# Kernel optimization log

Measured on AMD Instinct MI355X. Metric: run time of the kernel, lower is better.

## Reference

```python
import jax, jax.numpy as jnp
import numpy as np

# NTU RGB+D 25-joint skeleton edges (1-based)
NTU_EDGES = [(1,2),(2,21),(3,21),(4,3),(5,21),(6,5),(7,6),(8,7),(9,21),(10,9),
             (11,10),(12,11),(13,1),(14,13),(15,14),(16,15),(17,1),(18,17),
             (19,18),(20,19),(22,23),(23,8),(24,25),(25,12)]
NUM_SCALES = 13
NUM_POINT = 25


def build_A_powers(num_scales=NUM_SCALES, v=NUM_POINT):
    # MS-G3D disentangled multi-scale aggregation: exact-k-hop adjacencies, each
    # with self loops, symmetrically normalized, stacked along dim 0 -> (K*V, V).
    A = np.zeros((v, v))
    for i, j in NTU_EDGES:
        A[i - 1, j - 1] = 1.0
        A[j - 1, i - 1] = 1.0
    I = np.eye(v)
    mats = []
    for k in range(num_scales):
        if k == 0:
            Ak = I.copy()
        else:
            Ak = np.minimum(np.linalg.matrix_power(A + I, k), 1) \
               - np.minimum(np.linalg.matrix_power(A + I, k - 1), 1)
            Ak = Ak + I  # with_self=True
        d = Ak.sum(-1)
        dinv = np.where(d > 0, d ** -0.5, 0.0)
        mats.append((dinv[:, None] * Ak) * dinv[None, :])
    return np.concatenate(mats, 0).astype(np.float32)


def batchnorm(x, g, b, axes, ch_axis, eps=1e-5):
    # torch BatchNorm in training mode: biased batch stats + affine
    mean = jnp.mean(x, axes, keepdims=True)
    var = jnp.mean((x - mean) ** 2, axes, keepdims=True)
    shape = [1] * x.ndim
    shape[ch_axis] = -1
    return (x - mean) * jax.lax.rsqrt(var + eps) * g.reshape(shape) + b.reshape(shape)


def ms_gcn(x, A_powers, A_res, W, b, g, beta, num_scales):
    # x: (N, C, T, V); A: (K*V, V)
    A = A_powers + A_res
    support = jnp.einsum('vu,nctu->nctv', A, x)            # (N, C, T, K*V)
    N, C, T, KV = support.shape
    V = KV // num_scales
    support = support.reshape(N, C, T, num_scales, V).transpose(0, 3, 1, 2, 4)
    support = support.reshape(N, num_scales * C, T, V)     # (N, K*C, T, V)
    out = jnp.einsum('oc,nctv->notv', W, support) + b[None, :, None, None]  # 1x1 conv
    out = batchnorm(out, g, beta, (0, 2, 3), 1)
    return jax.nn.relu(out)


def lstm(x, Wih, Whh, bih, bhh):
    # single-layer batch_first LSTM, zero initial state; torch gate order i,f,g,o
    B = x.shape[0]
    H = Whh.shape[1]
    xp = jnp.einsum('bsd,hd->bsh', x, Wih) + bih + bhh     # precompute input proj

    def step(carry, xt):
        h, c = carry
        gates = xt + h @ Whh.T
        i, f, g, o = jnp.split(gates, 4, axis=-1)
        c = jax.nn.sigmoid(f) * c + jax.nn.sigmoid(i) * jnp.tanh(g)
        h = jax.nn.sigmoid(o) * jnp.tanh(c)
        return (h, c), h

    init = (jnp.zeros((B, H), x.dtype), jnp.zeros((B, H), x.dtype))
    _, ys = jax.lax.scan(step, init, jnp.swapaxes(xp, 0, 1))
    return jnp.swapaxes(ys, 0, 1)                          # (B, S, H)


def logsig_rnn(x, n_segments, Wih, Whh, bih, bhh):
    # x: (B, T, d). Depth-2 log-signature per time segment + segment start point,
    # concatenated and fed to an LSTM (Logsig-RNN layer).
    B, T, d = x.shape
    t_vec = np.array([int(round(float(v))) for v in np.linspace(1, T, n_segments + 1)])
    starts = t_vec[:-1] - 1
    ends = t_vec[1:] - 1
    L = int((ends - starts).max()) + 1
    # pad segments to fixed length by repeating the last point (zero increments)
    idx = np.minimum(starts[:, None] + np.arange(L)[None, :], ends[:, None])  # (S, L)
    pts = x[:, idx, :]                                     # (B, S, L, d)
    rel = pts - pts[:, :, :1, :]
    inc = rel[:, :, -1, :]                                 # level-1: total increment
    dx = pts[:, :, 1:, :] - pts[:, :, :-1, :]
    Mm = jnp.einsum('bsli,bslj->bsij', rel[:, :, :-1, :], dx)
    iu, ju = np.triu_indices(d, k=1)
    levy = 0.5 * (Mm[:, :, iu, ju] - Mm[:, :, ju, iu])     # level-2 (Lyndon basis)
    feats = jnp.concatenate([x[:, starts, :], inc, levy], axis=-1)
    return lstm(feats, Wih, Whh, bih, bhh)


def setup_inputs() -> dict:
    key = jax.random.key(0)
    ks = iter(jax.random.split(key, 16))
    N, C, T, V, M = 2, 3, 100, 25, 2
    c1, c2, num_class, K = 96, 192, 60, NUM_SCALES

    def randn(shape, scale):
        return jax.random.normal(next(ks), shape, jnp.float32) * scale

    ls1 = c1 + c1 * (c1 - 1) // 2     # 4656
    ls2 = c2 + c2 * (c2 - 1) // 2     # 18528
    in1 = c1 + ls1                    # 4752
    in2 = c2 + ls2                    # 18720
    Ap = jnp.asarray(build_A_powers())
    return {
        'x': jax.random.normal(next(ks), (N, C, T, V, M), jnp.float32),
        'length': jax.random.randint(next(ks), (N,), 0, T),
        'data_bn_g': jnp.ones((M * V * C,)), 'data_bn_b': jnp.zeros((M * V * C,)),
        'A_powers1': Ap,
        'A_res1': jax.random.uniform(next(ks), Ap.shape, jnp.float32, -1e-6, 1e-6),
        'W1': randn((c1, K * C), (K * C) ** -0.5), 'b1': jnp.zeros((c1,)),
        'bn1_g': jnp.ones((c1,)), 'bn1_b': jnp.zeros((c1,)),
        'Wih1': randn((4 * c1, in1), in1 ** -0.5), 'Whh1': randn((4 * c1, c1), c1 ** -0.5),
        'bih1': jnp.zeros((4 * c1,)), 'bhh1': jnp.zeros((4 * c1,)),
        'bnseg1_g': jnp.ones((50,)), 'bnseg1_b': jnp.zeros((50,)),
        'A_powers2': Ap,
        'A_res2': jax.random.uniform(next(ks), Ap.shape, jnp.float32, -1e-6, 1e-6),
        'W2': randn((c2, K * c1), (K * c1) ** -0.5), 'b2': jnp.zeros((c2,)),
        'bn2_g': jnp.ones((c2,)), 'bn2_b': jnp.zeros((c2,)),
        'Wih2': randn((4 * c2, in2), in2 ** -0.5), 'Whh2': randn((4 * c2, c2), c2 ** -0.5),
        'bih2': jnp.zeros((4 * c2,)), 'bhh2': jnp.zeros((4 * c2,)),
        'bnseg2_g': jnp.ones((30,)), 'bnseg2_b': jnp.zeros((30,)),
        'fcW': randn((num_class, c2), c2 ** -0.5), 'fcb': jnp.zeros((num_class,)),
    }


def reference(x, length, data_bn_g, data_bn_b, A_powers1, A_res1, W1, b1, bn1_g, bn1_b,
              Wih1, Whh1, bih1, bhh1, bnseg1_g, bnseg1_b, A_powers2, A_res2, W2, b2,
              bn2_g, bn2_b, Wih2, Whh2, bih2, bhh2, bnseg2_g, bnseg2_b, fcW, fcb):
    # `length` is accepted but unused, as in the original forward.
    N, C, T, V, M = x.shape
    K = A_powers1.shape[0] // V
    c1, c2 = W1.shape[0], W2.shape[0]
    S1, S2 = 50, 30

    h = x.transpose(0, 4, 3, 1, 2).reshape(N, M * V * C, T)
    h = batchnorm(h, data_bn_g, data_bn_b, (0, 2), 1)
    h = h.reshape(N * M, V, C, T).transpose(0, 2, 3, 1)            # (NM, C, T, V)

    h = jax.nn.relu(ms_gcn(h, A_powers1, A_res1, W1, b1, bn1_g, bn1_b, K))
    h = h.transpose(0, 3, 2, 1).reshape(N * M * V, T, c1)
    h = logsig_rnn(h, S1, Wih1, Whh1, bih1, bhh1)                  # (NMV, S1, c1)
    h = batchnorm(h, bnseg1_g, bnseg1_b, (0, 2), 1)
    h = h.reshape(N * M, V, S1, c1).transpose(0, 3, 2, 1)          # (NM, c1, S1, V)

    h = jax.nn.relu(ms_gcn(h, A_powers2, A_res2, W2, b2, bn2_g, bn2_b, K))
    h = h.transpose(0, 3, 2, 1).reshape(N * M * V, S1, c2)
    h = logsig_rnn(h, S2, Wih2, Whh2, bih2, bhh2)                  # (NMV, S2, c2)
    h = batchnorm(h, bnseg2_g, bnseg2_b, (0, 2), 1)
    h = h.reshape(N * M, V, S2, c2).transpose(0, 3, 2, 1)          # (NM, c2, S2, V)

    pooled = h.reshape(N, M, c2, -1).mean(axis=3).mean(axis=1)     # (N, c2)
    return pooled @ fcW.T + fcb
```

## Files before the change

kernel.cpp:

```cpp
#include <hip/hip_runtime.h>
#include <cmath>
#include <cstdint>
#include <cstddef>

typedef unsigned short bf16_t;
typedef __attribute__((ext_vector_type(8))) short short8;
typedef __attribute__((ext_vector_type(4))) float floatx4;
typedef __attribute__((ext_vector_type(2))) _Float16 half2_t;

__device__ __forceinline__ float bf2f(bf16_t b){
  unsigned int u = ((unsigned int)b) << 16;
  return __uint_as_float(u);
}
__device__ __forceinline__ bf16_t f2bf(float f){
  unsigned int u = __float_as_uint(f);
  unsigned int r = (u + 0x7fffu + ((u >> 16) & 1u)) >> 16;
  return (bf16_t)r;
}
__device__ __forceinline__ unsigned int f2bf2(float a, float b){
  return (unsigned int)f2bf(a) | ((unsigned int)f2bf(b) << 16);
}
__device__ __forceinline__ float sigf(float x){ return 1.0f / (1.0f + expf(-x)); }

__device__ __forceinline__ float dot2(half2_t a, half2_t b, float c){
#if __has_builtin(__builtin_amdgcn_fdot2)
  return __builtin_amdgcn_fdot2(a, b, c, false);
#else
  return c + (float)a.x * (float)b.x + (float)a.y * (float)b.y;
#endif
}

__device__ __forceinline__ void gload_lds16(const bf16_t* g, bf16_t* lds){
  __builtin_amdgcn_global_load_lds(
      (const __attribute__((address_space(1))) unsigned int*)g,
      (__attribute__((address_space(3))) unsigned int*)lds, 16, 0, 0);
}

__global__ void prep_misc(const float* __restrict__ a1, const float* __restrict__ r1, float* __restrict__ o1,
                          const float* __restrict__ a2, const float* __restrict__ r2, float* __restrict__ o2,
                          const float* __restrict__ bi1, const float* __restrict__ bh1, float* __restrict__ ob1,
                          const float* __restrict__ bi2, const float* __restrict__ bh2, float* __restrict__ ob2,
                          const float* __restrict__ Whh1, half2_t* __restrict__ Wp1,
                          const float* __restrict__ Whh2, half2_t* __restrict__ Wp2,
                          unsigned short* __restrict__ lut1, unsigned short* __restrict__ lut2,
                          float* __restrict__ stats, bf16_t* __restrict__ A2mat){
  int i = blockIdx.x * blockDim.x + threadIdx.x;
  if (i < 8125){ o1[i] = a1[i] + r1[i]; o2[i] = a2[i] + r2[i]; }
  if (i < 384) ob1[i] = bi1[i] + bh1[i];
  if (i < 768) ob2[i] = bi2[i] + bh2[i];
  if (i < 736) stats[i] = 0.f;
  if (i < 18432){
    int t = i % 384, j2 = i / 384;
    half2_t w; w.x = (_Float16)Whh1[(size_t)t * 96 + 2 * j2];
    w.y = (_Float16)Whh1[(size_t)t * 96 + 2 * j2 + 1];
    Wp1[i] = w;
  }
  if (i < 73728){
    int t = i % 768, j2 = i / 768;
    half2_t w; w.x = (_Float16)Whh2[(size_t)t * 192 + 2 * j2];
    w.y = (_Float16)Whh2[(size_t)t * 192 + 2 * j2 + 1];
    Wp2[i] = w;
  }
  if (i < 4560){
    int d = 96, p = i;
    int r = (int)(((2.0 * d - 1.0) - sqrt((2.0 * d - 1.0) * (2.0 * d - 1.0) - 8.0 * (double)p)) * 0.5);
    if (r < 0) r = 0;
    while (r + 1 <= d - 2 && (r + 1) * (d - 1) - ((r + 1) * r) / 2 <= p) ++r;
    while (r > 0 && r * (d - 1) - (r * (r - 1)) / 2 > p) --r;
    int jj = p - (r * (d - 1) - (r * (r - 1)) / 2);
    lut1[p] = (unsigned short)((r << 8) | (r + 1 + jj));
  }
  if (i < 18336){
    int d = 192, p = i;
    int r = (int)(((2.0 * d - 1.0) - sqrt((2.0 * d - 1.0) * (2.0 * d - 1.0) - 8.0 * (double)p)) * 0.5);
    if (r < 0) r = 0;
    while (r + 1 <= d - 2 && (r + 1) * (d - 1) - ((r + 1) * r) / 2 <= p) ++r;
    while (r > 0 && r * (d - 1) - (r * (r - 1)) / 2 > p) --r;
    int jj = p - (r * (d - 1) - (r * (r - 1)) / 2);
    lut2[p] = (unsigned short)((r << 8) | (r + 1 + jj));
  }
  if (i < 160000){
    int row = i >> 5, col = 1248 + (i & 31);
    A2mat[(size_t)row * 1280 + col] = 0;
  }
}

__device__ __forceinline__ void f2bf_seg(const float* in, bf16_t* out, int Kin, int Kout, int li){
  int ko8 = Kout >> 3;
  int r = li / ko8, k8 = (li % ko8) << 3;
  uint4 u;
  if (k8 + 8 <= Kin){
    const float4* p = reinterpret_cast<const float4*>(in + (size_t)r * Kin + k8);
    float4 x0 = p[0], x1 = p[1];
    u.x = f2bf2(x0.x, x0.y); u.y = f2bf2(x0.z, x0.w);
    u.z = f2bf2(x1.x, x1.y); u.w = f2bf2(x1.z, x1.w);
  } else {
    u.x = u.y = u.z = u.w = 0u;
  }
  *reinterpret_cast<uint4*>(out + (size_t)r * Kout + k8) = u;
}

__global__ void f2bf_pad8_3(const float* __restrict__ in1, bf16_t* __restrict__ out1, int Kin1, int Kout1, int c1,
                            const float* __restrict__ in2, bf16_t* __restrict__ out2, int Kin2, int Kout2, int c2,
                            const float* __restrict__ in3, bf16_t* __restrict__ out3, int Kin3, int Kout3, int c3){
  int idx = blockIdx.x * blockDim.x + threadIdx.x;
  if (idx < c1){ f2bf_seg(in1, out1, Kin1, Kout1, idx); return; }
  idx -= c1;
  if (idx < c2){ f2bf_seg(in2, out2, Kin2, Kout2, idx); return; }
  idx -= c2;
  if (idx < c3) f2bf_seg(in3, out3, Kin3, Kout3, idx);
}

__global__ void data_bn_kernel(const float* __restrict__ x, const float* __restrict__ g,
                               const float* __restrict__ bb, float* __restrict__ h1,
                               int N, int C, int T, int V, int M){
  int ch = blockIdx.x;
  int m = ch / (V * C);
  int v = (ch / C) % V;
  int c = ch % C;
  int tid = threadIdx.x;
  int cnt = N * T;
  float s = 0.f, s2 = 0.f;
  for (int i = tid; i < cnt; i += 64){
    int n = i / T, t = i % T;
    float val = x[(((size_t)(n * C + c) * T + t) * V + v) * M + m];
    s += val; s2 += val * val;
  }
  for (int off = 32; off; off >>= 1){ s += __shfl_down(s, off); s2 += __shfl_down(s2, off); }
  s = __shfl(s, 0); s2 = __shfl(s2, 0);
  float mean = s / cnt;
  float rstd = rsqrtf(s2 / cnt - mean * mean + 1e-5f);
  float gg = g[ch], bo = bb[ch];
  for (int i = tid; i < cnt; i += 64){
    int n = i / T, t = i % T;
    float val = x[(((size_t)(n * C + c) * T + t) * V + v) * M + m];
    float y = (val - mean) * rstd * gg + bo;
    h1[((size_t)((n * M + m) * C + c) * T + t) * V + v] = y;
  }
}

__global__ void support1_kernel(const float* __restrict__ A, const float* __restrict__ hin,
                                float* __restrict__ sup, int total){
  int idx = blockIdx.x * blockDim.x + threadIdx.x;
  if (idx >= total) return;
  int w = idx % 325;
  int rest = idx / 325;
  const float* row = hin + (size_t)rest * 25;
  const float* ar = A + w * 25;
  float acc = 0.f;
  #pragma unroll
  for (int u = 0; u < 25; ++u) acc += ar[u] * row[u];
  sup[idx] = acc;
}

__global__ void gcn1_out_kernel(const float* __restrict__ sup, const float* __restrict__ W1,
                                const float* __restrict__ b1, float* __restrict__ y1, int NM, int T){
  int idx = blockIdx.x * blockDim.x + threadIdx.x;
  int total = NM * T * 25 * 96;
  if (idx >= total) return;
  int o = idx % 96;
  int v = (idx / 96) % 25;
  int t = (idx / (96 * 25)) % T;
  int nm = idx / (96 * 25 * T);
  float acc = b1[o];
  #pragma unroll
  for (int k = 0; k < 13; ++k)
    #pragma unroll
    for (int c = 0; c < 3; ++c)
      acc += W1[o * 39 + k * 3 + c] * sup[(size_t)((nm * 3 + c) * T + t) * 325 + k * 25 + v];
  y1[idx] = acc;
}

__global__ void colstats_atomic(const float* __restrict__ mat, int R,
                                float* __restrict__ sum, float* __restrict__ sumsq){
  int col = threadIdx.x;
  int Cc = blockDim.x;
  float s = 0.f, s2 = 0.f;
  for (int r = blockIdx.x; r < R; r += gridDim.x){
    float v = mat[(size_t)r * Cc + col];
    s += v; s2 += v * v;
  }
  atomicAdd(&sum[col], s);
  atomicAdd(&sumsq[col], s2);
}

__global__ void segstats_atomic(const float* __restrict__ lout, int R2, int S,
                                float* __restrict__ sum, float* __restrict__ sumsq){
  int t = threadIdx.x;
  int H = blockDim.x;
  int nw = H >> 6;
  __shared__ float ra[4], rb[4];
  int lane = t & 63, wid = t >> 6;
  for (int r = blockIdx.x; r < R2; r += gridDim.x){
    int s = r % S;
    float v = lout[(size_t)r * H + t];
    float a = v, b2 = v * v;
    for (int off = 32; off; off >>= 1){ a += __shfl_down(a, off); b2 += __shfl_down(b2, off); }
    if (lane == 0){ ra[wid] = a; rb[wid] = b2; }
    __syncthreads();
    if (t == 0){
      float sa = 0.f, sb = 0.f;
      for (int w = 0; w < nw; ++w){ sa += ra[w]; sb += rb[w]; }
      atomicAdd(&sum[s], sa);
      atomicAdd(&sumsq[s], sb);
    }
    __syncthreads();
  }
}

__global__ void bn_relu_seq_kernel(const float* __restrict__ ymat, const float* __restrict__ sum,
                                   const float* __restrict__ sumsq, const float* __restrict__ g,
                                   const float* __restrict__ bb, float* __restrict__ xseq,
                                   int NM, int T, int H, int R){
  int idx = blockIdx.x * blockDim.x + threadIdx.x;
  int total = NM * T * 25 * H;
  if (idx >= total) return;
  int o = idx % H;
  int v = (idx / H) % 25;
  int t = (idx / (H * 25)) % T;
  int nm = idx / (H * 25 * T);
  float mean = sum[o] / R;
  float rstd = rsqrtf(sumsq[o] / R - mean * mean + 1e-5f);
  float val = (ymat[idx] - mean) * rstd * g[o] + bb[o];
  val = fmaxf(val, 0.f);
  int b = nm * 25 + v;
  xseq[((size_t)b * T + t) * H + o] = val;
}

struct SegTable { int st[50]; int en[50]; };

__global__ void feats_kernel(const float* __restrict__ xseq, bf16_t* __restrict__ feats,
                             SegTable segs, const unsigned int* __restrict__ lut32,
                             int T, int d, int S, int L, int pairs, int rowlenP){
  __shared__ float pts[4][192];
  int bs = blockIdx.x;
  int b = bs / S, s = bs % S;
  int st = segs.st[s], en = segs.en[s];
  int nt = blockDim.x, tid = threadIdx.x;
  for (int l = 0; l < L; ++l){
    int t = st + l; if (t > en) t = en;
    for (int i = tid; i < d; i += nt) pts[l][i] = xseq[((size_t)b * T + t) * d + i];
  }
  __syncthreads();
  unsigned int* frow32 = reinterpret_cast<unsigned int*>(feats + (size_t)bs * rowlenP);
  int d2 = d >> 1;
  for (int i2 = tid; i2 < d2; i2 += nt){
    int i = 2 * i2;
    frow32[i2]      = f2bf2(pts[0][i], pts[0][i + 1]);
    frow32[d2 + i2] = f2bf2(pts[L - 1][i] - pts[0][i], pts[L - 1][i + 1] - pts[0][i + 1]);
  }
  int rowlen2 = (2 * d + pairs) >> 1, rowlenP2 = rowlenP >> 1;
  for (int i = tid + rowlen2; i < rowlenP2; i += nt) frow32[i] = 0;
  int Lm2 = L - 2;
  unsigned int* lrow32 = frow32 + d;
  int pairs2 = pairs >> 1;
  for (int p2 = tid; p2 < pairs2; p2 += nt){
    unsigned int ee = lut32[p2];
    int i0 = (ee >> 8) & 255, j0 = ee & 255;
    int i1 = ee >> 24, j1 = (ee >> 16) & 255;
    float acc0 = 0.f, acc1 = 0.f;
    for (int l = 1; l <= Lm2; ++l){
      float p0i = pts[0][i0], p0j = pts[0][j0], p0i1 = pts[0][i1], p0j1 = pts[0][j1];
      float ri = pts[l][i0] - p0i, rj = pts[l][j0] - p0j;
      float di = pts[l + 1][i0] - pts[l][i0], dj = pts[l + 1][j0] - pts[l][j0];
      acc0 += ri * dj - rj * di;
      float ri1 = pts[l][i1] - p0i1, rj1 = pts[l][j1] - p0j1;
      float di1 = pts[l + 1][i1] - pts[l][i1], dj1 = pts[l + 1][j1] - pts[l][j1];
      acc1 += ri1 * dj1 - rj1 * di1;
    }
    lrow32[p2] = f2bf2(0.5f * acc0, 0.5f * acc1);
  }
}

__global__ __launch_bounds__(256)
void gemm_mfma_nt_split(const bf16_t* __restrict__ A, const bf16_t* __restrict__ B,
                        float* __restrict__ P, int M, int N, int K){
  __shared__ bf16_t As[128 * 64];
  __shared__ bf16_t Bs[128 * 64];
  const int tid = threadIdx.x;
  const int lane = tid & 63, wv = tid >> 6;
  const int bm = blockIdx.x * 128, bn = blockIdx.y * 128;
  const int wr = (wv >> 1) * 64, wc = (wv & 1) * 64;
  const int m_l = lane & 15, q = lane >> 4;

  const int ksteps = K >> 6;
  const int Z = gridDim.z, z = blockIdx.z;
  const int per = (ksteps + Z - 1) / Z;
  const int ks0 = z * per;
  const int ks1 = (ks0 + per < ksteps) ? ks0 + per : ksteps;

  const int rlane = lane >> 3;
  const int slane = lane & 7;
  const int colc = (slane ^ rlane) * 8;
  const bf16_t* gA[4]; const bf16_t* gB[4];
  bf16_t* lA[4]; bf16_t* lB[4];
  #pragma unroll
  for (int it = 0; it < 4; ++it){
    int c = it * 4 + wv;
    int rowA = bm + c * 8 + rlane; if (rowA > M - 1) rowA = M - 1;
    int rowB = bn + c * 8 + rlane; if (rowB > N - 1) rowB = N - 1;
    gA[it] = A + (size_t)rowA * K + colc;
    gB[it] = B + (size_t)rowB * K + colc;
    lA[it] = &As[c * 512];
    lB[it] = &Bs[c * 512];
  }
  const int sxor = m_l & 7;

  floatx4 acc[4][4] = {};
  for (int ks = ks0; ks < ks1; ++ks){
    int k0 = ks << 6;
    __syncthreads();
    #pragma unroll
    for (int it = 0; it < 4; ++it){
      gload_lds16(gA[it] + k0, lA[it]);
      gload_lds16(gB[it] + k0, lB[it]);
    }
    __syncthreads();
    #pragma unroll
    for (int half = 0; half < 2; ++half){
      const int scol = ((half * 4 + q) ^ sxor) * 8;
      short8 af[4], bfr[4];
      #pragma unroll
      for (int i = 0; i < 4; ++i){
        af[i]  = *reinterpret_cast<const short8*>(&As[(wr + i * 16 + m_l) * 64 + scol]);
        bfr[i] = *reinterpret_cast<const short8*>(&Bs[(wc + i * 16 + m_l) * 64 + scol]);
      }
      #pragma unroll
      for (int mi = 0; mi < 4; ++mi)
        #pragma unroll
        for (int ni = 0; ni < 4; ++ni)
          acc[mi][ni] = __builtin_amdgcn_mfma_f32_16x16x32_bf16(af[mi], bfr[ni], acc[mi][ni], 0, 0, 0);
    }
  }

  float* Pz = P + (size_t)z * M * N;
  #pragma unroll
  for (int mi = 0; mi < 4; ++mi){
    int row0 = bm + wr + mi * 16 + q * 4;
    #pragma unroll
    for (int r = 0; r < 4; ++r){
      int row = row0 + r;
      if (row < M){
        #pragma unroll
        for (int ni = 0; ni < 4; ++ni){
          int col = bn + wc + ni * 16 + m_l;
          if (col < N) Pz[(size_t)row * N + col] = acc[mi][ni][r];
        }
      }
    }
  }
}

__global__ void reduce_split_bias(const float* __restrict__ P, const float* __restrict__ bias,
                                  float* __restrict__ out, int MN, int N, int Z){
  int i4 = (blockIdx.x * blockDim.x + threadIdx.x) * 4;
  if (i4 >= MN) return;
  const float4 bv = *reinterpret_cast<const float4*>(bias + (i4 % N));
  float4 s = bv;
  for (int z = 0; z < Z; ++z){
    const float4 p = *reinterpret_cast<const float4*>(P + (size_t)z * MN + i4);
    s.x += p.x; s.y += p.y; s.z += p.z; s.w += p.w;
  }
  *reinterpret_cast<float4*>(out + i4) = s;
}

template <int H2C, int BLK, int Z>
__global__ __launch_bounds__(BLK)
void lstm_kernel(const float* __restrict__ P, const float* __restrict__ bias,
                 const half2_t* __restrict__ Wp, float* __restrict__ out,
                 int S, int MN){
  constexpr int H = 2 * H2C;
  constexpr int H4 = 4 * H;
  __shared__ _Float16 __attribute__((aligned(16))) hsh[H];
  __shared__ float gv[H4];
  const int b = blockIdx.x, t = threadIdx.x;
  half2_t w[H2C];
  const half2_t* wp = Wp + t;
  #pragma unroll
  for (int j2 = 0; j2 < H2C; ++j2) w[j2] = wp[(size_t)j2 * H4];
  float cc = 0.f;
  if (t < H) hsh[t] = (_Float16)0.f;
  const float bval = bias[t];
  const size_t base = (size_t)b * S * H4 + t;
  float pv0[Z], pv1[Z];
  #pragma unroll
  for (int z = 0; z < Z; ++z) pv0[z] = P[(size_t)z * MN + base];
  #pragma unroll
  for (int z = 0; z < Z; ++z) pv1[z] = P[(size_t)z * MN + base + H4];
  __syncthreads();
  const half2_t* hp = reinterpret_cast<const half2_t*>(hsh);
  for (int s = 0; s < S; ++s){
    float pvn[Z];
    if (s + 2 < S){
      size_t o2 = base + (size_t)(s + 2) * H4;
      #pragma unroll
      for (int z = 0; z < Z; ++z) pvn[z] = P[(size_t)z * MN + o2];
    }
    float a0 = bval, a1 = 0.f, a2 = 0.f, a3 = 0.f;
    float a4 = 0.f, a5 = 0.f, a6 = 0.f, a7 = 0.f;
    #pragma unroll
    for (int z = 0; z < Z; ++z) a0 += pv0[z];
    #pragma unroll
    for (int j2 = 0; j2 < H2C; j2 += 8){
      a0 = dot2(w[j2],     hp[j2],     a0);
      a1 = dot2(w[j2 + 1], hp[j2 + 1], a1);
      a2 = dot2(w[j2 + 2], hp[j2 + 2], a2);
      a3 = dot2(w[j2 + 3], hp[j2 + 3], a3);
      a4 = dot2(w[j2 + 4], hp[j2 + 4], a4);
      a5 = dot2(w[j2 + 5], hp[j2 + 5], a5);
      a6 = dot2(w[j2 + 6], hp[j2 + 6], a6);
      a7 = dot2(w[j2 + 7], hp[j2 + 7], a7);
    }
    gv[t] = ((a0 + a1) + (a2 + a3)) + ((a4 + a5) + (a6 + a7));
    __syncthreads();
    if (t < H){
      float ig = sigf(gv[t]);
      float fg = sigf(gv[H + t]);
      float gg = tanhf(gv[2 * H + t]);
      float og = sigf(gv[3 * H + t]);
      cc = fg * cc + ig * gg;
      float hh = og * tanhf(cc);
      hsh[t] = (_Float16)hh;
      out[((size_t)b * S + s) * H + t] = hh;
    }
    __syncthreads();
    #pragma unroll
    for (int z = 0; z < Z; ++z){ pv0[z] = pv1[z]; pv1[z] = pvn[z]; }
  }
}

__global__ void bnseg_to_g2in_kernel(const float* __restrict__ lout, const float* __restrict__ sum,
                                     const float* __restrict__ sumsq, const float* __restrict__ g,
                                     const float* __restrict__ bb, float* __restrict__ g2in,
                                     int B, int S, int H, int cnt){
  int idx = blockIdx.x * blockDim.x + threadIdx.x;
  int total = B * S * H;
  if (idx >= total) return;
  int hh = idx % H;
  int s = (idx / H) % S;
  int b = idx / (H * S);
  float mean = sum[s] / cnt;
  float rstd = rsqrtf(sumsq[s] / cnt - mean * mean + 1e-5f);
  float val = (lout[idx] - mean) * rstd * g[s] + bb[s];
  int nm = b / 25, v = b % 25;
  g2in[(((size_t)(nm * S + s) * 25 + v) * H) + hh] = val;
}

__global__ void support2_kernel(const float* __restrict__ A, const float* __restrict__ g2in,
                                bf16_t* __restrict__ A2mat, int NM, int C1, int S){
  int idx = blockIdx.x * blockDim.x + threadIdx.x;
  int total = NM * S * 25 * 13 * 96;
  if (idx >= total) return;
  int c = idx % 96;
  int k = (idx / 96) % 13;
  int v = (idx / (96 * 13)) % 25;
  int rs = idx / (96 * 13 * 25);
  const float* gbase = g2in + ((size_t)rs * 25) * 96 + c;
  const float* ar = A + (k * 25 + v) * 25;
  float acc = 0.f;
  #pragma unroll
  for (int u = 0; u < 25; ++u) acc += ar[u] * gbase[(size_t)u * 96];
  A2mat[((size_t)rs * 25 + v) * 1280 + k * 96 + c] = f2bf(acc);
}

__global__ void pool_kernel(const float* __restrict__ lout2, const float* __restrict__ sum,
                            const float* __restrict__ sumsq, const float* __restrict__ g,
                            const float* __restrict__ bb, float* __restrict__ pooled,
                            int S, int H, int scnt){
  int n = blockIdx.x / H;
  int o = blockIdx.x % H;
  float acc = 0.f;
  int cnt = 2 * 25 * S;
  for (int i = threadIdx.x; i < cnt; i += 64){
    int m = i / (25 * S);
    int r = i % (25 * S);
    int v = r / S;
    int s = r % S;
    int b = (n * 2 + m) * 25 + v;
    float val = lout2[((size_t)b * S + s) * H + o];
    float mean = sum[s] / scnt;
    float rstd = rsqrtf(sumsq[s] / scnt - mean * mean + 1e-5f);
    val = (val - mean) * rstd * g[s] + bb[s];
    acc += val;
  }
  for (int off = 32; off; off >>= 1) acc += __shfl_down(acc, off);
  if (threadIdx.x == 0) pooled[n * H + o] = acc / cnt;
}

__global__ void fc_kernel(const float* __restrict__ pooled, const float* __restrict__ fcW,
                          const float* __restrict__ fcb, float* __restrict__ outp){
  int idx = blockIdx.x * blockDim.x + threadIdx.x;
  if (idx >= 120) return;
  int n = idx / 60, cls = idx % 60;
  float acc = fcb[cls];
  for (int o = 0; o < 192; ++o) acc += pooled[n * 192 + o] * fcW[cls * 192 + o];
  outp[idx] = acc;
}

static void make_segs(int T, int S, SegTable& tab, int& L){
  double step = (double)(T - 1) / (double)S;
  long long tv[51];
  for (int i = 0; i <= S; ++i){
    double v = 1.0 + step * (double)i;
    tv[i] = llrint(v);
  }
  L = 0;
  for (int s = 0; s < S; ++s){
    tab.st[s] = (int)tv[s] - 1;
    tab.en[s] = (int)tv[s + 1] - 1;
    int len = tab.en[s] - tab.st[s] + 1;
    if (len > L) L = len;
  }
  for (int s = S; s < 50; ++s){ tab.st[s] = 0; tab.en[s] = 0; }
  if (L > 4) L = 4;
}

extern "C" void kernel_launch(void* const* d_in, const int* in_sizes, int n_in,
                              void* d_out, int out_size, void* d_ws, size_t ws_size,
                              hipStream_t stream){
  const float* x         = (const float*)d_in[0];
  const float* data_bn_g = (const float*)d_in[2];
  const float* data_bn_b = (const float*)d_in[3];
  const float* A_powers1 = (const float*)d_in[4];
  const float* A_res1    = (const float*)d_in[5];
  const float* W1        = (const float*)d_in[6];
  const float* b1        = (const float*)d_in[7];
  const float* bn1_g     = (const float*)d_in[8];
  const float* bn1_b     = (const float*)d_in[9];
  const float* Wih1      = (const float*)d_in[10];
  const float* Whh1      = (const float*)d_in[11];
  const float* bih1      = (const float*)d_in[12];
  const float* bhh1      = (const float*)d_in[13];
  const float* bnseg1_g  = (const float*)d_in[14];
  const float* bnseg1_b  = (const float*)d_in[15];
  const float* A_powers2 = (const float*)d_in[16];
  const float* A_res2    = (const float*)d_in[17];
  const float* W2        = (const float*)d_in[18];
  const float* b2        = (const float*)d_in[19];
  const float* bn2_g     = (const float*)d_in[20];
  const float* bn2_b     = (const float*)d_in[21];
  const float* Wih2      = (const float*)d_in[22];
  const float* Whh2      = (const float*)d_in[23];
  const float* bih2      = (const float*)d_in[24];
  const float* bhh2      = (const float*)d_in[25];
  const float* bnseg2_g  = (const float*)d_in[26];
  const float* bnseg2_b  = (const float*)d_in[27];
  const float* fcW       = (const float*)d_in[28];
  const float* fcb       = (const float*)d_in[29];
  float* out = (float*)d_out;

  const int N = 2, C = 3, T = 100, V = 25, M = 2, NM = 4;
  const int K = 13, C1 = 96, C2 = 192;
  const int S1 = 50, S2 = 30;
  const int B = 100;
  const int IN1 = 4752, IN2 = 18720;
  const int IN1P = 4800, IN2P = 18752;
  const int P1 = 4560, P2 = 18336;
  const int KG2 = 1248, KG2P = 1280;
  const int Z1 = 5, Z2 = 6, ZG = 4;

  size_t off = 0;
  char* base = (char*)d_ws;
  auto alloc = [&](size_t nbytes) -> void* {
    off = (off + 255) & ~(size_t)255;
    void* p = base + off;
    off += nbytes;
    return p;
  };
  float* A1full = (float*)alloc(325 * 25 * 4);
  float* A2full = (float*)alloc(325 * 25 * 4);
  float* h1     = (float*)alloc((size_t)NM * C * T * V * 4);
  float* sup1   = (float*)alloc((size_t)NM * C * T * 325 * 4);
  float* y1mat  = (float*)alloc((size_t)NM * T * V * C1 * 4);
  float* stats  = (float*)alloc(736 * 4);
  float* st1a = stats, *st1b = stats + 96;
  float* sg1a = stats + 192, *sg1b = stats + 242;
  float* st2a = stats + 292, *st2b = stats + 484;
  float* sg2a = stats + 676, *sg2b = stats + 706;
  float* xseq1  = (float*)alloc((size_t)B * T * C1 * 4);
  float* l1out  = (float*)alloc((size_t)B * S1 * C1 * 4);
  float* g2in   = (float*)alloc((size_t)NM * S1 * V * C1 * 4);
  bf16_t* A2mat = (bf16_t*)alloc((size_t)NM * S1 * V * KG2P * 2);
  float* y2mat  = (float*)alloc((size_t)NM * S1 * V * C2 * 4);
  float* xseq2  = (float*)alloc((size_t)B * S1 * C2 * 4);
  float* l2out  = (float*)alloc((size_t)B * S2 * C2 * 4);
  float* pooled = (float*)alloc(2 * C2 * 4);
  float* bias1  = (float*)alloc(4 * C1 * 4);
  float* bias2  = (float*)alloc(4 * C2 * 4);
  half2_t* Wp1  = (half2_t*)alloc((size_t)(C1 / 2) * 4 * C1 * 4);
  half2_t* Wp2  = (half2_t*)alloc((size_t)(C2 / 2) * 4 * C2 * 4);
  bf16_t* Wih1b = (bf16_t*)alloc((size_t)4 * C1 * IN1P * 2);
  bf16_t* Wih2b = (bf16_t*)alloc((size_t)4 * C2 * IN2P * 2);
  bf16_t* W2b   = (bf16_t*)alloc((size_t)C2 * KG2P * 2);
  unsigned short* lut1 = (unsigned short*)alloc((size_t)P1 * 2);
  unsigned short* lut2 = (unsigned short*)alloc((size_t)P2 * 2);
  size_t pmax = (size_t)Z2 * 3000 * 768;
  {
    size_t p1s = (size_t)Z1 * 5000 * 384; if (p1s > pmax) pmax = p1s;
    size_t pgs = (size_t)ZG * 5000 * 192; if (pgs > pmax) pmax = pgs;
  }
  float* Pbuf = (float*)alloc(pmax * 4);
  bf16_t* feats = (bf16_t*)alloc((size_t)B * S2 * IN2P * 2);
  (void)ws_size; (void)in_sizes; (void)n_in; (void)out_size;

  prep_misc<<<625, 256, 0, stream>>>(A_powers1, A_res1, A1full, A_powers2, A_res2, A2full,
                                     bih1, bhh1, bias1, bih2, bhh2, bias2,
                                     Whh1, Wp1, Whh2, Wp2, lut1, lut2, stats, A2mat);
  {
    int c1 = 4 * C1 * (IN1P / 8);
    int c2 = 4 * C2 * (IN2P / 8);
    int c3 = C2 * (KG2P / 8);
    int tot = c1 + c2 + c3;
    f2bf_pad8_3<<<(tot + 255) / 256, 256, 0, stream>>>(Wih1, Wih1b, IN1, IN1P, c1,
                                                       Wih2, Wih2b, IN2, IN2P, c2,
                                                       W2, W2b, KG2, KG2P, c3);
  }

  data_bn_kernel<<<M * V * C, 64, 0, stream>>>(x, data_bn_g, data_bn_b, h1, N, C, T, V, M);

  int tot_sup1 = NM * C * T * 325;
  support1_kernel<<<(tot_sup1 + 255) / 256, 256, 0, stream>>>(A1full, h1, sup1, tot_sup1);
  int tot_y1 = NM * T * 25 * C1;
  gcn1_out_kernel<<<(tot_y1 + 255) / 256, 256, 0, stream>>>(sup1, W1, b1, y1mat, NM, T);
  colstats_atomic<<<256, C1, 0, stream>>>(y1mat, NM * T * 25, st1a, st1b);
  bn_relu_seq_kernel<<<(tot_y1 + 255) / 256, 256, 0, stream>>>(y1mat, st1a, st1b, bn1_g, bn1_b,
                                                               xseq1, NM, T, C1, NM * T * 25);

  SegTable seg1, seg2; int L1, L2;
  make_segs(T, S1, seg1, L1);
  make_segs(S1, S2, seg2, L2);

  feats_kernel<<<B * S1, 256, 0, stream>>>(xseq1, feats, seg1, (const unsigned int*)lut1,
                                           T, C1, S1, L1, P1, IN1P);
  {
    int Mm = B * S1, Nn = 4 * C1;
    dim3 g((Mm + 127) / 128, (Nn + 127) / 128, Z1);
    gemm_mfma_nt_split<<<g, 256, 0, stream>>>(feats, Wih1b, Pbuf, Mm, Nn, IN1P);
    lstm_kernel<48, 384, Z1><<<B, 384, 0, stream>>>(Pbuf, bias1, Wp1, l1out, S1, Mm * Nn);
  }
  segstats_atomic<<<256, C1, 0, stream>>>(l1out, B * S1, S1, sg1a, sg1b);
  int tot_bn1 = B * S1 * C1;
  bnseg_to_g2in_kernel<<<(tot_bn1 + 255) / 256, 256, 0, stream>>>(l1out, sg1a, sg1b, bnseg1_g,
                                                                  bnseg1_b, g2in, B, S1, C1, B * C1);

  int tot_sup2 = NM * S1 * 25 * 13 * 96;
  support2_kernel<<<(tot_sup2 + 255) / 256, 256, 0, stream>>>(A2full, g2in, A2mat, NM, C1, S1);
  {
    int Mm = NM * S1 * 25, Nn = C2;
    dim3 g((Mm + 127) / 128, (Nn + 127) / 128, ZG);
    gemm_mfma_nt_split<<<g, 256, 0, stream>>>(A2mat, W2b, Pbuf, Mm, Nn, KG2P);
    int MN = Mm * Nn;
    reduce_split_bias<<<(MN / 4 + 255) / 256, 256, 0, stream>>>(Pbuf, b2, y2mat, MN, Nn, ZG);
  }
  colstats_atomic<<<256, C2, 0, stream>>>(y2mat, NM * S1 * 25, st2a, st2b);
  int tot_y2 = NM * S1 * 25 * C2;
  bn_relu_seq_kernel<<<(tot_y2 + 255) / 256, 256, 0, stream>>>(y2mat, st2a, st2b, bn2_g, bn2_b,
                                                               xseq2, NM, S1, C2, NM * S1 * 25);

  feats_kernel<<<B * S2, 256, 0, stream>>>(xseq2, feats, seg2, (const unsigned int*)lut2,
                                           S1, C2, S2, L2, P2, IN2P);
  {
    int Mm = B * S2, Nn = 4 * C2;
    dim3 g((Mm + 127) / 128, (Nn + 127) / 128, Z2);
    gemm_mfma_nt_split<<<g, 256, 0, stream>>>(feats, Wih2b, Pbuf, Mm, Nn, IN2P);
    lstm_kernel<96, 768, Z2><<<B, 768, 0, stream>>>(Pbuf, bias2, Wp2, l2out, S2, Mm * Nn);
  }
  segstats_atomic<<<256, C2, 0, stream>>>(l2out, B * S2, S2, sg2a, sg2b);

  pool_kernel<<<2 * C2, 64, 0, stream>>>(l2out, sg2a, sg2b, bnseg2_g, bnseg2_b, pooled, S2, C2, B * C2);
  fc_kernel<<<1, 128, 0, stream>>>(pooled, fcW, fcb, out);
}
```

Before: 706.7 us.

## Fuse GCN, batchnorm stats and weight conversion into neighbouring kernels

Merges support1, gcn1_out and its column stats into one per-(nm,t) block kernel. Folds the BN+ReLU application into the feature kernel, the segment stats into the LSTM step loop, and the segment BN into support2. Moves the fp32-to-bf16 weight conversion into the GEMM B-tile load, and computes GCN2 stats during the split-K reduction. The aim is to cut many launches and intermediate buffers, at the cost of redundant per-call weight conversion inside the GEMM and extra shared atomics.

```diff
diff --git a/kernel.cpp b/kernel.cpp
--- a/kernel.cpp
+++ b/kernel.cpp
@@ -85,32 +85,6 @@
   }
 }
 
-__device__ __forceinline__ void f2bf_seg(const float* in, bf16_t* out, int Kin, int Kout, int li){
-  int ko8 = Kout >> 3;
-  int r = li / ko8, k8 = (li % ko8) << 3;
-  uint4 u;
-  if (k8 + 8 <= Kin){
-    const float4* p = reinterpret_cast<const float4*>(in + (size_t)r * Kin + k8);
-    float4 x0 = p[0], x1 = p[1];
-    u.x = f2bf2(x0.x, x0.y); u.y = f2bf2(x0.z, x0.w);
-    u.z = f2bf2(x1.x, x1.y); u.w = f2bf2(x1.z, x1.w);
-  } else {
-    u.x = u.y = u.z = u.w = 0u;
-  }
-  *reinterpret_cast<uint4*>(out + (size_t)r * Kout + k8) = u;
-}
-
-__global__ void f2bf_pad8_3(const float* __restrict__ in1, bf16_t* __restrict__ out1, int Kin1, int Kout1, int c1,
-                            const float* __restrict__ in2, bf16_t* __restrict__ out2, int Kin2, int Kout2, int c2,
-                            const float* __restrict__ in3, bf16_t* __restrict__ out3, int Kin3, int Kout3, int c3){
-  int idx = blockIdx.x * blockDim.x + threadIdx.x;
-  if (idx < c1){ f2bf_seg(in1, out1, Kin1, Kout1, idx); return; }
-  idx -= c1;
-  if (idx < c2){ f2bf_seg(in2, out2, Kin2, Kout2, idx); return; }
-  idx -= c2;
-  if (idx < c3) f2bf_seg(in3, out3, Kin3, Kout3, idx);
-}
-
 __global__ void data_bn_kernel(const float* __restrict__ x, const float* __restrict__ g,
                                const float* __restrict__ bb, float* __restrict__ h1,
                                int N, int C, int T, int V, int M){
@@ -139,107 +113,68 @@
   }
 }
 
-__global__ void support1_kernel(const float* __restrict__ A, const float* __restrict__ hin,
-                                float* __restrict__ sup, int total){
-  int idx = blockIdx.x * blockDim.x + threadIdx.x;
-  if (idx >= total) return;
-  int w = idx % 325;
-  int rest = idx / 325;
-  const float* row = hin + (size_t)rest * 25;
-  const float* ar = A + w * 25;
-  float acc = 0.f;
-  #pragma unroll
-  for (int u = 0; u < 25; ++u) acc += ar[u] * row[u];
-  sup[idx] = acc;
-}
-
-__global__ void gcn1_out_kernel(const float* __restrict__ sup, const float* __restrict__ W1,
-                                const float* __restrict__ b1, float* __restrict__ y1, int NM, int T){
-  int idx = blockIdx.x * blockDim.x + threadIdx.x;
-  int total = NM * T * 25 * 96;
-  if (idx >= total) return;
-  int o = idx % 96;
-  int v = (idx / 96) % 25;
-  int t = (idx / (96 * 25)) % T;
-  int nm = idx / (96 * 25 * T);
-  float acc = b1[o];
-  #pragma unroll
-  for (int k = 0; k < 13; ++k)
-    #pragma unroll
-    for (int c = 0; c < 3; ++c)
-      acc += W1[o * 39 + k * 3 + c] * sup[(size_t)((nm * 3 + c) * T + t) * 325 + k * 25 + v];
-  y1[idx] = acc;
-}
-
-__global__ void colstats_atomic(const float* __restrict__ mat, int R,
-                                float* __restrict__ sum, float* __restrict__ sumsq){
-  int col = threadIdx.x;
-  int Cc = blockDim.x;
-  float s = 0.f, s2 = 0.f;
-  for (int r = blockIdx.x; r < R; r += gridDim.x){
-    float v = mat[(size_t)r * Cc + col];
-    s += v; s2 += v * v;
-  }
-  atomicAdd(&sum[col], s);
-  atomicAdd(&sumsq[col], s2);
-}
-
-__global__ void segstats_atomic(const float* __restrict__ lout, int R2, int S,
-                                float* __restrict__ sum, float* __restrict__ sumsq){
-  int t = threadIdx.x;
-  int H = blockDim.x;
-  int nw = H >> 6;
-  __shared__ float ra[4], rb[4];
-  int lane = t & 63, wid = t >> 6;
-  for (int r = blockIdx.x; r < R2; r += gridDim.x){
-    int s = r % S;
-    float v = lout[(size_t)r * H + t];
-    float a = v, b2 = v * v;
-    for (int off = 32; off; off >>= 1){ a += __shfl_down(a, off); b2 += __shfl_down(b2, off); }
-    if (lane == 0){ ra[wid] = a; rb[wid] = b2; }
-    __syncthreads();
-    if (t == 0){
-      float sa = 0.f, sb = 0.f;
-      for (int w = 0; w < nw; ++w){ sa += ra[w]; sb += rb[w]; }
-      atomicAdd(&sum[s], sa);
-      atomicAdd(&sumsq[s], sb);
-    }
-    __syncthreads();
-  }
-}
-
-__global__ void bn_relu_seq_kernel(const float* __restrict__ ymat, const float* __restrict__ sum,
-                                   const float* __restrict__ sumsq, const float* __restrict__ g,
-                                   const float* __restrict__ bb, float* __restrict__ xseq,
-                                   int NM, int T, int H, int R){
-  int idx = blockIdx.x * blockDim.x + threadIdx.x;
-  int total = NM * T * 25 * H;
-  if (idx >= total) return;
-  int o = idx % H;
-  int v = (idx / H) % 25;
-  int t = (idx / (H * 25)) % T;
-  int nm = idx / (H * 25 * T);
-  float mean = sum[o] / R;
-  float rstd = rsqrtf(sumsq[o] / R - mean * mean + 1e-5f);
-  float val = (ymat[idx] - mean) * rstd * g[o] + bb[o];
-  val = fmaxf(val, 0.f);
-  int b = nm * 25 + v;
-  xseq[((size_t)b * T + t) * H + o] = val;
+__global__ __launch_bounds__(256)
+void gcn1_fused(const float* __restrict__ A, const float* __restrict__ h1,
+                const float* __restrict__ W1, const float* __restrict__ b1,
+                float* __restrict__ y1, float* __restrict__ ssum, float* __restrict__ ssq, int T){
+  __shared__ float h[3][25];
+  __shared__ float sup[3][325];
+  __shared__ float lsum[96], lsq[96];
+  int blk = blockIdx.x;
+  int nm = blk / T, t = blk % T;
+  int tid = threadIdx.x;
+  if (tid < 75){
+    int c = tid / 25, v = tid % 25;
+    h[c][v] = h1[((size_t)(nm * 3 + c) * T + t) * 25 + v];
+  }
+  if (tid < 96){ lsum[tid] = 0.f; lsq[tid] = 0.f; }
+  __syncthreads();
+  for (int w = tid; w < 975; w += 256){
+    int c = w / 325, ww = w % 325;
+    const float* ar = A + ww * 25;
+    float acc = 0.f;
+    #pragma unroll
+    for (int u = 0; u < 25; ++u) acc += ar[u] * h[c][u];
+    sup[c][ww] = acc;
+  }
+  __syncthreads();
+  for (int o2 = tid; o2 < 2400; o2 += 256){
+    int v = o2 / 96, o = o2 % 96;
+    float acc = b1[o];
+    #pragma unroll
+    for (int k = 0; k < 13; ++k)
+      #pragma unroll
+      for (int c = 0; c < 3; ++c)
+        acc += W1[o * 39 + k * 3 + c] * sup[c][k * 25 + v];
+    y1[((size_t)blk * 25 + v) * 96 + o] = acc;
+    atomicAdd(&lsum[o], acc);
+    atomicAdd(&lsq[o], acc * acc);
+  }
+  __syncthreads();
+  if (tid < 96){ atomicAdd(&ssum[tid], lsum[tid]); atomicAdd(&ssq[tid], lsq[tid]); }
 }
 
 struct SegTable { int st[50]; int en[50]; };
 
-__global__ void feats_kernel(const float* __restrict__ xseq, bf16_t* __restrict__ feats,
-                             SegTable segs, const unsigned int* __restrict__ lut32,
-                             int T, int d, int S, int L, int pairs, int rowlenP){
+__global__ void feats_bn_kernel(const float* __restrict__ ymat, const float* __restrict__ sum,
+                                const float* __restrict__ sumsq, const float* __restrict__ g,
+                                const float* __restrict__ bb, bf16_t* __restrict__ feats,
+                                SegTable segs, const unsigned int* __restrict__ lut32,
+                                int T, int d, int S, int L, int pairs, int rowlenP, int R){
   __shared__ float pts[4][192];
   int bs = blockIdx.x;
   int b = bs / S, s = bs % S;
+  int nm = b / 25, v = b % 25;
   int st = segs.st[s], en = segs.en[s];
   int nt = blockDim.x, tid = threadIdx.x;
   for (int l = 0; l < L; ++l){
     int t = st + l; if (t > en) t = en;
-    for (int i = tid; i < d; i += nt) pts[l][i] = xseq[((size_t)b * T + t) * d + i];
+    const float* yrow = ymat + ((size_t)(nm * T + t) * 25 + v) * d;
+    for (int i = tid; i < d; i += nt){
+      float mean = sum[i] / R;
+      float rstd = rsqrtf(sumsq[i] / R - mean * mean + 1e-5f);
+      pts[l][i] = fmaxf((yrow[i] - mean) * rstd * g[i] + bb[i], 0.f);
+    }
   }
   __syncthreads();
   unsigned int* frow32 = reinterpret_cast<unsigned int*>(feats + (size_t)bs * rowlenP);
@@ -260,11 +195,10 @@
     int i1 = ee >> 24, j1 = (ee >> 16) & 255;
     float acc0 = 0.f, acc1 = 0.f;
     for (int l = 1; l <= Lm2; ++l){
-      float p0i = pts[0][i0], p0j = pts[0][j0], p0i1 = pts[0][i1], p0j1 = pts[0][j1];
-      float ri = pts[l][i0] - p0i, rj = pts[l][j0] - p0j;
+      float ri = pts[l][i0] - pts[0][i0], rj = pts[l][j0] - pts[0][j0];
       float di = pts[l + 1][i0] - pts[l][i0], dj = pts[l + 1][j0] - pts[l][j0];
       acc0 += ri * dj - rj * di;
-      float ri1 = pts[l][i1] - p0i1, rj1 = pts[l][j1] - p0j1;
+      float ri1 = pts[l][i1] - pts[0][i1], rj1 = pts[l][j1] - pts[0][j1];
       float di1 = pts[l + 1][i1] - pts[l][i1], dj1 = pts[l + 1][j1] - pts[l][j1];
       acc1 += ri1 * dj1 - rj1 * di1;
     }
@@ -273,8 +207,8 @@
 }
 
 __global__ __launch_bounds__(256)
-void gemm_mfma_nt_split(const bf16_t* __restrict__ A, const bf16_t* __restrict__ B,
-                        float* __restrict__ P, int M, int N, int K){
+void gemm_mfma_f32b(const bf16_t* __restrict__ A, const float* __restrict__ B,
+                    float* __restrict__ P, int M, int N, int K, int Kb){
   __shared__ bf16_t As[128 * 64];
   __shared__ bf16_t Bs[128 * 64];
   const int tid = threadIdx.x;
@@ -292,28 +226,41 @@
   const int rlane = lane >> 3;
   const int slane = lane & 7;
   const int colc = (slane ^ rlane) * 8;
-  const bf16_t* gA[4]; const bf16_t* gB[4];
-  bf16_t* lA[4]; bf16_t* lB[4];
+  const bf16_t* gA[4];
+  const float* gBf[4];
+  bf16_t* lA[4];
+  bf16_t* lB[4];
   #pragma unroll
   for (int it = 0; it < 4; ++it){
     int c = it * 4 + wv;
     int rowA = bm + c * 8 + rlane; if (rowA > M - 1) rowA = M - 1;
     int rowB = bn + c * 8 + rlane; if (rowB > N - 1) rowB = N - 1;
     gA[it] = A + (size_t)rowA * K + colc;
-    gB[it] = B + (size_t)rowB * K + colc;
+    gBf[it] = B + (size_t)rowB * Kb;
     lA[it] = &As[c * 512];
-    lB[it] = &Bs[c * 512];
+    lB[it] = &Bs[c * 512 + (size_t)lane * 8];
   }
   const int sxor = m_l & 7;
 
   floatx4 acc[4][4] = {};
   for (int ks = ks0; ks < ks1; ++ks){
     int k0 = ks << 6;
+    int kk = k0 + colc;
     __syncthreads();
     #pragma unroll
+    for (int it = 0; it < 4; ++it) gload_lds16(gA[it] + k0, lA[it]);
+    #pragma unroll
     for (int it = 0; it < 4; ++it){
-      gload_lds16(gA[it] + k0, lA[it]);
-      gload_lds16(gB[it] + k0, lB[it]);
+      uint4 u;
+      if (kk + 8 <= Kb){
+        const float4* p = reinterpret_cast<const float4*>(gBf[it] + kk);
+        float4 x0 = p[0], x1 = p[1];
+        u.x = f2bf2(x0.x, x0.y); u.y = f2bf2(x0.z, x0.w);
+        u.z = f2bf2(x1.x, x1.y); u.w = f2bf2(x1.z, x1.w);
+      } else {
+        u.x = u.y = u.z = u.w = 0u;
+      }
+      *reinterpret_cast<uint4*>(lB[it]) = u;
     }
     __syncthreads();
     #pragma unroll
@@ -351,29 +298,46 @@
   }
 }
 
-__global__ void reduce_split_bias(const float* __restrict__ P, const float* __restrict__ bias,
-                                  float* __restrict__ out, int MN, int N, int Z){
-  int i4 = (blockIdx.x * blockDim.x + threadIdx.x) * 4;
-  if (i4 >= MN) return;
-  const float4 bv = *reinterpret_cast<const float4*>(bias + (i4 % N));
-  float4 s = bv;
-  for (int z = 0; z < Z; ++z){
-    const float4 p = *reinterpret_cast<const float4*>(P + (size_t)z * MN + i4);
-    s.x += p.x; s.y += p.y; s.z += p.z; s.w += p.w;
-  }
-  *reinterpret_cast<float4*>(out + i4) = s;
+__global__ __launch_bounds__(256)
+void reduce_split_bias_stats(const float* __restrict__ P, const float* __restrict__ bias,
+                             float* __restrict__ out, float* __restrict__ ssum, float* __restrict__ ssq,
+                             int MN, int N, int Z){
+  __shared__ float lsum[192], lsq[192];
+  int tid = threadIdx.x;
+  if (tid < 192){ lsum[tid] = 0.f; lsq[tid] = 0.f; }
+  __syncthreads();
+  int i4 = (blockIdx.x * blockDim.x + tid) * 4;
+  if (i4 < MN){
+    const float4 bv = *reinterpret_cast<const float4*>(bias + (i4 % N));
+    float4 s = bv;
+    for (int z = 0; z < Z; ++z){
+      const float4 p = *reinterpret_cast<const float4*>(P + (size_t)z * MN + i4);
+      s.x += p.x; s.y += p.y; s.z += p.z; s.w += p.w;
+    }
+    *reinterpret_cast<float4*>(out + i4) = s;
+    int c0 = i4 % N;
+    atomicAdd(&lsum[c0],     s.x); atomicAdd(&lsq[c0],     s.x * s.x);
+    atomicAdd(&lsum[c0 + 1], s.y); atomicAdd(&lsq[c0 + 1], s.y * s.y);
+    atomicAdd(&lsum[c0 + 2], s.z); atomicAdd(&lsq[c0 + 2], s.z * s.z);
+    atomicAdd(&lsum[c0 + 3], s.w); atomicAdd(&lsq[c0 + 3], s.w * s.w);
+  }
+  __syncthreads();
+  if (tid < 192){ atomicAdd(&ssum[tid], lsum[tid]); atomicAdd(&ssq[tid], lsq[tid]); }
 }
 
 template <int H2C, int BLK, int Z>
 __global__ __launch_bounds__(BLK)
 void lstm_kernel(const float* __restrict__ P, const float* __restrict__ bias,
                  const half2_t* __restrict__ Wp, float* __restrict__ out,
+                 float* __restrict__ ssum, float* __restrict__ ssq,
                  int S, int MN){
   constexpr int H = 2 * H2C;
   constexpr int H4 = 4 * H;
   __shared__ _Float16 __attribute__((aligned(16))) hsh[H];
   __shared__ float gv[H4];
+  __shared__ float ra[BLK / 64], rb[BLK / 64];
   const int b = blockIdx.x, t = threadIdx.x;
+  const int lane = t & 63, wid = t >> 6;
   half2_t w[H2C];
   const half2_t* wp = Wp + t;
   #pragma unroll
@@ -413,6 +377,7 @@
     }
     gv[t] = ((a0 + a1) + (a2 + a3)) + ((a4 + a5) + (a6 + a7));
     __syncthreads();
+    float gvv = 0.f;
     if (t < H){
       float ig = sigf(gv[t]);
       float fg = sigf(gv[H + t]);
@@ -422,44 +387,47 @@
       float hh = og * tanhf(cc);
       hsh[t] = (_Float16)hh;
       out[((size_t)b * S + s) * H + t] = hh;
-    }
+      gvv = hh;
+    }
+    float q1 = gvv, q2 = gvv * gvv;
+    for (int off2 = 32; off2; off2 >>= 1){ q1 += __shfl_down(q1, off2); q2 += __shfl_down(q2, off2); }
+    if (lane == 0){ ra[wid] = q1; rb[wid] = q2; }
     __syncthreads();
+    if (t == 0){
+      float sa = 0.f, sb = 0.f;
+      #pragma unroll
+      for (int ww = 0; ww < BLK / 64; ++ww){ sa += ra[ww]; sb += rb[ww]; }
+      atomicAdd(&ssum[s], sa);
+      atomicAdd(&ssq[s], sb);
+    }
     #pragma unroll
     for (int z = 0; z < Z; ++z){ pv0[z] = pv1[z]; pv1[z] = pvn[z]; }
   }
 }
 
-__global__ void bnseg_to_g2in_kernel(const float* __restrict__ lout, const float* __restrict__ sum,
-                                     const float* __restrict__ sumsq, const float* __restrict__ g,
-                                     const float* __restrict__ bb, float* __restrict__ g2in,
-                                     int B, int S, int H, int cnt){
+__global__ void support2_bn(const float* __restrict__ A, const float* __restrict__ lout,
+                            const float* __restrict__ ssum, const float* __restrict__ ssq,
+                            const float* __restrict__ g, const float* __restrict__ bb,
+                            bf16_t* __restrict__ A2mat, int S, int cnt){
   int idx = blockIdx.x * blockDim.x + threadIdx.x;
-  int total = B * S * H;
-  if (idx >= total) return;
-  int hh = idx % H;
-  int s = (idx / H) % S;
-  int b = idx / (H * S);
-  float mean = sum[s] / cnt;
-  float rstd = rsqrtf(sumsq[s] / cnt - mean * mean + 1e-5f);
-  float val = (lout[idx] - mean) * rstd * g[s] + bb[s];
-  int nm = b / 25, v = b % 25;
-  g2in[(((size_t)(nm * S + s) * 25 + v) * H) + hh] = val;
-}
-
-__global__ void support2_kernel(const float* __restrict__ A, const float* __restrict__ g2in,
-                                bf16_t* __restrict__ A2mat, int NM, int C1, int S){
-  int idx = blockIdx.x * blockDim.x + threadIdx.x;
-  int total = NM * S * 25 * 13 * 96;
+  int total = 4 * S * 25 * 13 * 96;
   if (idx >= total) return;
   int c = idx % 96;
   int k = (idx / 96) % 13;
   int v = (idx / (96 * 13)) % 25;
   int rs = idx / (96 * 13 * 25);
-  const float* gbase = g2in + ((size_t)rs * 25) * 96 + c;
+  int s = rs % S, nm = rs / S;
+  float mean = ssum[s] / cnt;
+  float rstd = rsqrtf(ssq[s] / cnt - mean * mean + 1e-5f);
+  float scale = rstd * g[s];
+  float shift = bb[s] - mean * scale;
   const float* ar = A + (k * 25 + v) * 25;
   float acc = 0.f;
   #pragma unroll
-  for (int u = 0; u < 25; ++u) acc += ar[u] * gbase[(size_t)u * 96];
+  for (int u = 0; u < 25; ++u){
+    float raw = lout[((size_t)(nm * 25 + u) * S + s) * 96 + c];
+    acc += ar[u] * (raw * scale + shift);
+  }
   A2mat[((size_t)rs * 25 + v) * 1280 + k * 96 + c] = f2bf(acc);
 }
 
@@ -550,7 +518,7 @@
   float* out = (float*)d_out;
 
   const int N = 2, C = 3, T = 100, V = 25, M = 2, NM = 4;
-  const int K = 13, C1 = 96, C2 = 192;
+  const int C1 = 96, C2 = 192;
   const int S1 = 50, S2 = 30;
   const int B = 100;
   const int IN1 = 4752, IN2 = 18720;
@@ -570,28 +538,21 @@
   float* A1full = (float*)alloc(325 * 25 * 4);
   float* A2full = (float*)alloc(325 * 25 * 4);
   float* h1     = (float*)alloc((size_t)NM * C * T * V * 4);
-  float* sup1   = (float*)alloc((size_t)NM * C * T * 325 * 4);
   float* y1mat  = (float*)alloc((size_t)NM * T * V * C1 * 4);
   float* stats  = (float*)alloc(736 * 4);
   float* st1a = stats, *st1b = stats + 96;
   float* sg1a = stats + 192, *sg1b = stats + 242;
   float* st2a = stats + 292, *st2b = stats + 484;
   float* sg2a = stats + 676, *sg2b = stats + 706;
-  float* xseq1  = (float*)alloc((size_t)B * T * C1 * 4);
   float* l1out  = (float*)alloc((size_t)B * S1 * C1 * 4);
-  float* g2in   = (float*)alloc((size_t)NM * S1 * V * C1 * 4);
   bf16_t* A2mat = (bf16_t*)alloc((size_t)NM * S1 * V * KG2P * 2);
   float* y2mat  = (float*)alloc((size_t)NM * S1 * V * C2 * 4);
-  float* xseq2  = (float*)alloc((size_t)B * S1 * C2 * 4);
   float* l2out  = (float*)alloc((size_t)B * S2 * C2 * 4);
   float* pooled = (float*)alloc(2 * C2 * 4);
   float* bias1  = (float*)alloc(4 * C1 * 4);
   float* bias2  = (float*)alloc(4 * C2 * 4);
   half2_t* Wp1  = (half2_t*)alloc((size_t)(C1 / 2) * 4 * C1 * 4);
   half2_t* Wp2  = (half2_t*)alloc((size_t)(C2 / 2) * 4 * C2 * 4);
-  bf16_t* Wih1b = (bf16_t*)alloc((size_t)4 * C1 * IN1P * 2);
-  bf16_t* Wih2b = (bf16_t*)alloc((size_t)4 * C2 * IN2P * 2);
-  bf16_t* W2b   = (bf16_t*)alloc((size_t)C2 * KG2P * 2);
   unsigned short* lut1 = (unsigned short*)alloc((size_t)P1 * 2);
   unsigned short* lut2 = (unsigned short*)alloc((size_t)P2 * 2);
   size_t pmax = (size_t)Z2 * 3000 * 768;
@@ -606,66 +567,48 @@
   prep_misc<<<625, 256, 0, stream>>>(A_powers1, A_res1, A1full, A_powers2, A_res2, A2full,
                                      bih1, bhh1, bias1, bih2, bhh2, bias2,
                                      Whh1, Wp1, Whh2, Wp2, lut1, lut2, stats, A2mat);
-  {
-    int c1 = 4 * C1 * (IN1P / 8);
-    int c2 = 4 * C2 * (IN2P / 8);
-    int c3 = C2 * (KG2P / 8);
-    int tot = c1 + c2 + c3;
-    f2bf_pad8_3<<<(tot + 255) / 256, 256, 0, stream>>>(Wih1, Wih1b, IN1, IN1P, c1,
-                                                       Wih2, Wih2b, IN2, IN2P, c2,
-                                                       W2, W2b, KG2, KG2P, c3);
-  }
 
   data_bn_kernel<<<M * V * C, 64, 0, stream>>>(x, data_bn_g, data_bn_b, h1, N, C, T, V, M);
 
-  int tot_sup1 = NM * C * T * 325;
-  support1_kernel<<<(tot_sup1 + 255) / 256, 256, 0, stream>>>(A1full, h1, sup1, tot_sup1);
-  int tot_y1 = NM * T * 25 * C1;
-  gcn1_out_kernel<<<(tot_y1 + 255) / 256, 256, 0, stream>>>(sup1, W1, b1, y1mat, NM, T);
-  colstats_atomic<<<256, C1, 0, stream>>>(y1mat, NM * T * 25, st1a, st1b);
-  bn_relu_seq_kernel<<<(tot_y1 + 255) / 256, 256, 0, stream>>>(y1mat, st1a, st1b, bn1_g, bn1_b,
-                                                               xseq1, NM, T, C1, NM * T * 25);
+  gcn1_fused<<<NM * T, 256, 0, stream>>>(A1full, h1, W1, b1, y1mat, st1a, st1b, T);
 
   SegTable seg1, seg2; int L1, L2;
   make_segs(T, S1, seg1, L1);
   make_segs(S1, S2, seg2, L2);
 
-  feats_kernel<<<B * S1, 256, 0, stream>>>(xseq1, feats, seg1, (const unsigned int*)lut1,
-                                           T, C1, S1, L1, P1, IN1P);
+  feats_bn_kernel<<<B * S1, 256, 0, stream>>>(y1mat, st1a, st1b, bn1_g, bn1_b, feats, seg1,
+                                              (const unsigned int*)lut1, T, C1, S1, L1, P1, IN1P,
+                                              NM * T * 25);
   {
     int Mm = B * S1, Nn = 4 * C1;
     dim3 g((Mm + 127) / 128, (Nn + 127) / 128, Z1);
-    gemm_mfma_nt_split<<<g, 256, 0, stream>>>(feats, Wih1b, Pbuf, Mm, Nn, IN1P);
-    lstm_kernel<48, 384, Z1><<<B, 384, 0, stream>>>(Pbuf, bias1, Wp1, l1out, S1, Mm * Nn);
-  }
-  segstats_atomic<<<256, C1, 0, stream>>>(l1out, B * S1, S1, sg1a, sg1b);
-  int tot_bn1 = B * S1 * C1;
-  bnseg_to_g2in_kernel<<<(tot_bn1 + 255) / 256, 256, 0, stream>>>(l1out, sg1a, sg1b, bnseg1_g,
-                                                                  bnseg1_b, g2in, B, S1, C1, B * C1);
-
-  int tot_sup2 = NM * S1 * 25 * 13 * 96;
-  support2_kernel<<<(tot_sup2 + 255) / 256, 256, 0, stream>>>(A2full, g2in, A2mat, NM, C1, S1);
+    gemm_mfma_f32b<<<g, 256, 0, stream>>>(feats, Wih1, Pbuf, Mm, Nn, IN1P, IN1);
+    lstm_kernel<48, 384, Z1><<<B, 384, 0, stream>>>(Pbuf, bias1, Wp1, l1out, sg1a, sg1b, S1, Mm * Nn);
+  }
+
+  {
+    int tot = NM * S1 * 25 * 13 * 96;
+    support2_bn<<<(tot + 255) / 256, 256, 0, stream>>>(A2full, l1out, sg1a, sg1b, bnseg1_g,
+                                                       bnseg1_b, A2mat, S1, B * C1);
+  }
   {
     int Mm = NM * S1 * 25, Nn = C2;
     dim3 g((Mm + 127) / 128, (Nn + 127) / 128, ZG);
-    gemm_mfma_nt_split<<<g, 256, 0, stream>>>(A2mat, W2b, Pbuf, Mm, Nn, KG2P);
+    gemm_mfma_f32b<<<g, 256, 0, stream>>>(A2mat, W2, Pbuf, Mm, Nn, KG2P, KG2);
     int MN = Mm * Nn;
-    reduce_split_bias<<<(MN / 4 + 255) / 256, 256, 0, stream>>>(Pbuf, b2, y2mat, MN, Nn, ZG);
-  }
-  colstats_atomic<<<256, C2, 0, stream>>>(y2mat, NM * S1 * 25, st2a, st2b);
-  int tot_y2 = NM * S1 * 25 * C2;
-  bn_relu_seq_kernel<<<(tot_y2 + 255) / 256, 256, 0, stream>>>(y2mat, st2a, st2b, bn2_g, bn2_b,
-                                                               xseq2, NM, S1, C2, NM * S1 * 25);
-
-  feats_kernel<<<B * S2, 256, 0, stream>>>(xseq2, feats, seg2, (const unsigned int*)lut2,
-                                           S1, C2, S2, L2, P2, IN2P);
+    reduce_split_bias_stats<<<(MN / 4 + 255) / 256, 256, 0, stream>>>(Pbuf, b2, y2mat, st2a, st2b,
+                                                                      MN, Nn, ZG);
+  }
+
+  feats_bn_kernel<<<B * S2, 256, 0, stream>>>(y2mat, st2a, st2b, bn2_g, bn2_b, feats, seg2,
+                                              (const unsigned int*)lut2, S1, C2, S2, L2, P2, IN2P,
+                                              NM * S1 * 25);
   {
     int Mm = B * S2, Nn = 4 * C2;
     dim3 g((Mm + 127) / 128, (Nn + 127) / 128, Z2);
-    gemm_mfma_nt_split<<<g, 256, 0, stream>>>(feats, Wih2b, Pbuf, Mm, Nn, IN2P);
-    lstm_kernel<96, 768, Z2><<<B, 768, 0, stream>>>(Pbuf, bias2, Wp2, l2out, S2, Mm * Nn);
-  }
-  segstats_atomic<<<256, C2, 0, stream>>>(l2out, B * S2, S2, sg2a, sg2b);
+    gemm_mfma_f32b<<<g, 256, 0, stream>>>(feats, Wih2, Pbuf, Mm, Nn, IN2P, IN2);
+    lstm_kernel<96, 768, Z2><<<B, 768, 0, stream>>>(Pbuf, bias2, Wp2, l2out, sg2a, sg2b, S2, Mm * Nn);
+  }
 
   pool_kernel<<<2 * C2, 64, 0, stream>>>(l2out, sg2a, sg2b, bnseg2_g, bnseg2_b, pooled, S2, C2, B * C2);
   fc_kernel<<<1, 128, 0, stream>>>(pooled, fcW, fcb, out);
```

After: 783.0 us. +10.8%, slower.
